# Kernel optimization log

Hardware: AMD Instinct MI355X
Metric: run time of the kernel (lower is better)

Reference implementation:

```python
import jax, jax.numpy as jnp
import numpy as np

B, T, D = 8, 1024, 1024
H = 16
HD = D // H
FF = 4 * D
EPS = 1e-5


def _ln(x, gamma, beta):
    # torch.var default is unbiased (ddof=1); MyLayerNorm intended normalization
    mean = jnp.mean(x, axis=-1, keepdims=True)
    var = jnp.var(x, axis=-1, keepdims=True, ddof=1)
    return (x - mean) / jnp.sqrt(var + EPS) * gamma + beta


def setup_inputs() -> dict:
    key = jax.random.key(0)
    ks = jax.random.split(key, 16)
    s = lambda k, shape, fan: jax.random.normal(k, shape, jnp.float32) * (fan ** -0.5)
    return {
        "x": jax.random.normal(ks[0], (B, T, D), jnp.float32),
        "Wq": s(ks[1], (D, D), D), "bq": jnp.zeros((D,), jnp.float32),
        "Wk": s(ks[2], (D, D), D), "bk": jnp.zeros((D,), jnp.float32),
        "Wv": s(ks[3], (D, D), D), "bv": jnp.zeros((D,), jnp.float32),
        "Wo": s(ks[4], (D, D), D), "bo": jnp.zeros((D,), jnp.float32),
        "W1": s(ks[5], (D, FF), D), "b1": jnp.zeros((FF,), jnp.float32),
        "W2": s(ks[6], (FF, D), FF), "b2": jnp.zeros((D,), jnp.float32),
        "g1": jnp.ones((D,), jnp.float32), "be1": jnp.zeros((D,), jnp.float32),
        "g2": jnp.ones((D,), jnp.float32), "be2": jnp.zeros((D,), jnp.float32),
    }


def reference(x, Wq, bq, Wk, bk, Wv, bv, Wo, bo, W1, b1, W2, b2, g1, be1, g2, be2):
    # pre-attention LN
    h = _ln(x, g1, be1)
    # batched QKV (equivalent to concatenated per-head Linears)
    q = (h @ Wq + bq).reshape(B, T, H, HD)
    k = (h @ Wk + bk).reshape(B, T, H, HD)
    v = (h @ Wv + bv).reshape(B, T, H, HD)
    att = jnp.einsum("bthd,bshd->bhts", q, k) * (HD ** -0.5)
    att = jax.nn.softmax(att, axis=-1)
    ctx = jnp.einsum("bhts,bshd->bthd", att, v).reshape(B, T, D)
    h = h + (ctx @ Wo + bo)
    # pre-FFN LN
    h2 = _ln(h, g2, be2)
    ff = jax.nn.gelu(h2 @ W1 + b1, approximate=False) @ W2 + b2
    return h2 + ff
```

## Files before the change

### kernel.cpp

```cpp
#include <hip/hip_runtime.h>
#include <hip/hip_bf16.h>

typedef unsigned short u16;
typedef __attribute__((ext_vector_type(8))) short bf16x8;
typedef __attribute__((ext_vector_type(4))) float floatx4;

__device__ __forceinline__ u16 f2b(float f) {
    union { float f; unsigned int u; } a; a.f = f;
    unsigned int u = a.u;
    unsigned int r = (u + 0x7fffu + ((u >> 16) & 1u)) >> 16;
    return (u16)r;
}
__device__ __forceinline__ float b2f(u16 v) {
    union { unsigned int u; float f; } a; a.u = ((unsigned int)v) << 16;
    return a.f;
}
__device__ __forceinline__ unsigned int cvt_pk_bf16(float lo, float hi) {
    unsigned int r;
    asm("v_cvt_pk_bf16_f32 %0, %1, %2" : "=v"(r) : "v"(lo), "v"(hi));
    return r;
}

__device__ __forceinline__ void gload_lds16(const void* g, void* l) {
    auto gp = (const __attribute__((address_space(1))) unsigned int*)g;
    auto lp = (__attribute__((address_space(3))) unsigned int*)l;
    __builtin_amdgcn_global_load_lds(gp, lp, 16, 0, 0);
}

__global__ __launch_bounds__(256) void k_ln_bf(const float* __restrict__ x,
                                               const float* __restrict__ g,
                                               const float* __restrict__ be,
                                               u16* __restrict__ yb) {
    const int row = blockIdx.x;
    const int t = threadIdx.x;
    const float4 xv = ((const float4*)(x + (size_t)row * 1024))[t];
    float s  = xv.x + xv.y + xv.z + xv.w;
    float ss = xv.x * xv.x + xv.y * xv.y + xv.z * xv.z + xv.w * xv.w;
    for (int m = 1; m < 64; m <<= 1) {
        s  += __shfl_xor(s, m);
        ss += __shfl_xor(ss, m);
    }
    __shared__ float sm[8];
    const int wave = t >> 6, lane = t & 63;
    if (lane == 0) { sm[wave] = s; sm[4 + wave] = ss; }
    __syncthreads();
    s  = sm[0] + sm[1] + sm[2] + sm[3];
    ss = sm[4] + sm[5] + sm[6] + sm[7];
    const float mean = s * (1.0f / 1024.0f);
    const float var  = (ss - 1024.0f * mean * mean) * (1.0f / 1023.0f);
    const float rstd = rsqrtf(var + 1e-5f);
    const float4 gv = ((const float4*)g)[t];
    const float4 bv = ((const float4*)be)[t];
    float4 y;
    y.x = (xv.x - mean) * rstd * gv.x + bv.x;
    y.y = (xv.y - mean) * rstd * gv.y + bv.y;
    y.z = (xv.z - mean) * rstd * gv.z + bv.z;
    y.w = (xv.w - mean) * rstd * gv.w + bv.w;
    uint2 pk;
    pk.x = (unsigned int)f2b(y.x) | ((unsigned int)f2b(y.y) << 16);
    pk.y = (unsigned int)f2b(y.z) | ((unsigned int)f2b(y.w) << 16);
    *(uint2*)(yb + (size_t)row * 1024 + t * 4) = pk;
}

__global__ __launch_bounds__(256) void k_tconv(const float* __restrict__ W,
                                               u16* __restrict__ Wt,
                                               int K, int N) {
    __shared__ float tile[32][33];
    const int n0 = blockIdx.x * 32, k0 = blockIdx.y * 32;
    const int tx = threadIdx.x, ty = threadIdx.y;
    for (int i = 0; i < 4; i++) {
        const int kr = ty + i * 8;
        tile[kr][tx] = W[(size_t)(k0 + kr) * N + n0 + tx];
    }
    __syncthreads();
    for (int i = 0; i < 4; i++) {
        const int nr = ty + i * 8;
        Wt[(size_t)(n0 + nr) * K + k0 + tx] = f2b(tile[tx][nr]);
    }
}

__global__ __launch_bounds__(256) void k_tconv4(const float* __restrict__ s0, u16* __restrict__ d0,
                                                const float* __restrict__ s1, u16* __restrict__ d1,
                                                const float* __restrict__ s2, u16* __restrict__ d2,
                                                const float* __restrict__ s3, u16* __restrict__ d3) {
    __shared__ float tile[32][33];
    const float* W; u16* Wt;
    switch (blockIdx.z) {
        case 0: W = s0; Wt = d0; break;
        case 1: W = s1; Wt = d1; break;
        case 2: W = s2; Wt = d2; break;
        default: W = s3; Wt = d3; break;
    }
    const int n0 = blockIdx.x * 32, k0 = blockIdx.y * 32;
    const int tx = threadIdx.x, ty = threadIdx.y;
    for (int i = 0; i < 4; i++) {
        const int kr = ty + i * 8;
        tile[kr][tx] = W[(size_t)(k0 + kr) * 1024 + n0 + tx];
    }
    __syncthreads();
    for (int i = 0; i < 4; i++) {
        const int nr = ty + i * 8;
        Wt[(size_t)(n0 + nr) * 1024 + k0 + tx] = f2b(tile[tx][nr]);
    }
}

__global__ __launch_bounds__(256) void k_vtrans(const u16* __restrict__ v,
                                                u16* __restrict__ vt) {
    __shared__ u16 tile[64][80];
    const int t = threadIdx.x;
    const int t0 = blockIdx.x * 64, hh = blockIdx.y, bb = blockIdx.z;
    const int r = t >> 2, c0 = (t & 3) * 16;
    const u16* src = v + ((size_t)(bb * 1024 + t0 + r)) * 1024 + hh * 64 + c0;
    *(uint4*)&tile[r][c0]     = *(const uint4*)src;
    *(uint4*)&tile[r][c0 + 8] = *(const uint4*)(src + 8);
    __syncthreads();
    const int d = t >> 2;
    u16* dst = vt + (((size_t)(bb * 16 + hh) * 64 + d)) * 1024 + t0 + c0;
    union { u16 s[8]; uint4 v4; } pk;
    for (int j = 0; j < 8; j++) pk.s[j] = tile[c0 + j][d];
    *(uint4*)dst = pk.v4;
    for (int j = 0; j < 8; j++) pk.s[j] = tile[c0 + 8 + j][d];
    *(uint4*)(dst + 8) = pk.v4;
}

template <bool GELU, bool RESID, bool WF32, bool WBF16, bool QKV = false>
__global__ __launch_bounds__(256) void k_gemm(const u16* __restrict__ A,
                                              const u16* __restrict__ Bt,
                                              const float* __restrict__ bias,
                                              const u16* __restrict__ residB,
                                              float* __restrict__ outF,
                                              u16* __restrict__ outB,
                                              int M, int N, int K,
                                              const float* __restrict__ bias2 = nullptr,
                                              const float* __restrict__ bias3 = nullptr) {
    __shared__ __align__(16) u16 S[16896];
    u16* As = S;
    u16* Bs = S + 8192;
    const int t = threadIdx.x;

    const int nb = gridDim.x;
    const int linear = blockIdx.y * nb + blockIdx.x;
    const int per = nb * 8;
    const int gg = linear / per, rr = linear % per;
    const int m0 = (gg * 8 + (rr & 7)) * 128;
    const int n0 = (rr >> 3) * 128;

    const int lane = t & 63, wave = t >> 6;
    const int wm = (wave >> 1) * 64, wn = (wave & 1) * 64;
    const int r16 = lane & 15, quad = lane >> 4;

    floatx4 acc[4][4];
    const floatx4 zero = {0.0f, 0.0f, 0.0f, 0.0f};
    for (int i = 0; i < 4; i++)
        for (int j = 0; j < 4; j++) acc[i][j] = zero;

    const u16* pa[4];
    const u16* pb[4];
    #pragma unroll
    for (int i = 0; i < 4; i++) {
        const int L = t + i * 256;
        const int row = L >> 3, col = L & 7;
        const int gcol = col ^ (row & 7);
        pa[i] = A  + (size_t)(m0 + row) * K + gcol * 8;
        pb[i] = Bt + (size_t)(n0 + row) * K + gcol * 8;
    }

    for (int kk = 0; kk < K; kk += 64) {
        #pragma unroll
        for (int i = 0; i < 4; i++) {
            gload_lds16(pa[i] + kk, As + (t + i * 256) * 8);
            gload_lds16(pb[i] + kk, Bs + (t + i * 256) * 8);
        }
        __syncthreads();

        #pragma unroll
        for (int ks = 0; ks < 2; ks++) {
            bf16x8 af[4], bfr[4];
            #pragma unroll
            for (int i = 0; i < 4; i++) {
                const int ra = wm + i * 16 + r16;
                af[i] = *(const bf16x8*)(As + ra * 64 + (((ks << 2) + quad) ^ (ra & 7)) * 8);
                const int rb = wn + i * 16 + r16;
                bfr[i] = *(const bf16x8*)(Bs + rb * 64 + (((ks << 2) + quad) ^ (rb & 7)) * 8);
            }
            #pragma unroll
            for (int mi = 0; mi < 4; mi++)
                #pragma unroll
                for (int ni = 0; ni < 4; ni++)
                    acc[mi][ni] = __builtin_amdgcn_mfma_f32_16x16x32_bf16(af[mi], bfr[ni], acc[mi][ni], 0, 0, 0);
        }
        __syncthreads();
    }

    const int sect = QKV ? (n0 >> 10) : 0;
    const float* bp = QKV ? (sect == 0 ? bias : (sect == 1 ? bias2 : bias3)) : bias;
    u16* outQ = QKV ? (outB + (size_t)sect * (8192ull * 1024ull)) : outB;

    if (WBF16) {
        u16 (*ct)[132] = (u16(*)[132])S;
        for (int mi = 0; mi < 4; mi++)
            for (int ni = 0; ni < 4; ni++) {
                const int col = wn + ni * 16 + r16;
                const int coln = QKV ? ((n0 + col) & 1023) : (n0 + col);
                const float bv = bp[coln];
                for (int r = 0; r < 4; r++) {
                    const int row = wm + mi * 16 + quad * 4 + r;
                    float v = acc[mi][ni][r] + bv;
                    if (GELU) v = 0.5f * v * (1.0f + erff(v * 0.70710678118654752f));
                    ct[row][col] = f2b(v);
                }
            }
        __syncthreads();
        const int orow = t >> 1, oc = (t & 1) * 64;
        const int grow = m0 + orow;
        u16* dst = QKV ? (outQ + (size_t)grow * 1024 + ((n0 + oc) & 1023))
                       : (outB + (size_t)grow * N + n0 + oc);
        #pragma unroll
        for (int j = 0; j < 8; j++)
            *(uint4*)(dst + j * 8) = *(const uint4*)&ct[orow][oc + j * 8];
    } else {
        for (int mi = 0; mi < 4; mi++)
            for (int ni = 0; ni < 4; ni++) {
                const int gcol = n0 + wn + ni * 16 + r16;
                const float bv = bias[gcol];
                for (int r = 0; r < 4; r++) {
                    const int grow = m0 + wm + mi * 16 + quad * 4 + r;
                    float v = acc[mi][ni][r] + bv;
                    if (GELU) v = 0.5f * v * (1.0f + erff(v * 0.70710678118654752f));
                    const size_t o = (size_t)grow * N + gcol;
                    if (RESID) v += b2f(residB[o]);
                    if (WF32) outF[o] = v;
                }
            }
    }
}

__global__ __launch_bounds__(256) void k_attn_mfma(const u16* __restrict__ q,
                                                   const u16* __restrict__ k,
                                                   const u16* __restrict__ vt,
                                                   u16* __restrict__ ctx) {
    __shared__ u16 Ks[2][64][40];
    __shared__ u16 Vs[2][64][40];
    __shared__ u16 Ps[2][64][40];
    const int t = threadIdx.x;
    const int lane = t & 63, wave = t >> 6;
    const int r16 = lane & 15, quad = lane >> 4;
    const int wq = wave * 16;
    const int bx = blockIdx.x;
    const int qt = bx & 15, hh = (bx >> 4) & 15, bb = bx >> 8;
    const size_t qk_base = ((size_t)bb * 1024) * 1024 + hh * 64;
    const size_t vt_base = ((size_t)(bb * 16 + hh) * 64) * 1024;
    const int q0 = qt * 64;
    const float C1 = 0.18033688011112042f;

    bf16x8 qf[2];
    {
        const u16* qp = q + qk_base + (size_t)(q0 + wq + r16) * 1024 + quad * 8;
        qf[0] = *(const bf16x8*)qp;
        qf[1] = *(const bf16x8*)(qp + 32);
    }

    const int srow = t >> 2, ch = t & 3;
    const int pnl = ch >> 1, soff = (ch & 1) * 16;
    const u16* gkb = k + qk_base + (size_t)srow * 1024 + ch * 16;
    const u16* gvb = vt + vt_base + (size_t)srow * 1024 + ch * 16;

    uint4 k0v = *(const uint4*)gkb;
    uint4 k1v = *(const uint4*)(gkb + 8);
    uint4 v0v = *(const uint4*)gvb;
    uint4 v1v = *(const uint4*)(gvb + 8);

    float m_i = -INFINITY, l_i = 0.0f;
    floatx4 acc_o[4];
    const floatx4 zero = {0.0f, 0.0f, 0.0f, 0.0f};
    for (int ni = 0; ni < 4; ni++) acc_o[ni] = zero;

    for (int st = 0; st < 16; st++) {
        *(uint4*)&Ks[pnl][srow][soff]     = k0v;
        *(uint4*)&Ks[pnl][srow][soff + 8] = k1v;
        *(uint4*)&Vs[pnl][srow][soff]     = v0v;
        *(uint4*)&Vs[pnl][srow][soff + 8] = v1v;
        __syncthreads();

        const int sn = (st + 1) & 15;
        const u16* gk = gkb + (size_t)sn * 65536;
        const u16* gv = gvb + sn * 64;
        const uint4 kn0 = *(const uint4*)gk;
        const uint4 kn1 = *(const uint4*)(gk + 8);
        const uint4 vn0 = *(const uint4*)gv;
        const uint4 vn1 = *(const uint4*)(gv + 8);

        floatx4 accs[4];
        for (int ni = 0; ni < 4; ni++) accs[ni] = zero;
        #pragma unroll
        for (int ks = 0; ks < 2; ks++) {
            #pragma unroll
            for (int ni = 0; ni < 4; ni++) {
                const bf16x8 kf = *(const bf16x8*)&Ks[ks][ni * 16 + r16][quad * 8];
                accs[ni] = __builtin_amdgcn_mfma_f32_16x16x32_bf16(kf, qf[ks], accs[ni], 0, 0, 0);
            }
        }

        float mx = -INFINITY;
        #pragma unroll
        for (int ni = 0; ni < 4; ni++)
            #pragma unroll
            for (int r = 0; r < 4; r++) mx = fmaxf(mx, accs[ni][r]);
        mx = fmaxf(mx, __shfl_xor(mx, 16));
        mx = fmaxf(mx, __shfl_xor(mx, 32));
        const float mn = fmaxf(m_i, mx);
        const float al = exp2f((m_i - mn) * C1);
        m_i = mn;
        const float negmc = -mn * C1;
        float ps = 0.0f;
        #pragma unroll
        for (int ni = 0; ni < 4; ni++) {
            const float p0 = exp2f(fmaf(accs[ni][0], C1, negmc));
            const float p1 = exp2f(fmaf(accs[ni][1], C1, negmc));
            const float p2 = exp2f(fmaf(accs[ni][2], C1, negmc));
            const float p3 = exp2f(fmaf(accs[ni][3], C1, negmc));
            ps += (p0 + p1) + (p2 + p3);
            uint2 w;
            w.x = cvt_pk_bf16(p0, p1);
            w.y = cvt_pk_bf16(p2, p3);
            *(uint2*)&Ps[ni >> 1][wq + r16][(ni & 1) * 16 + quad * 4] = w;
        }
        ps += __shfl_xor(ps, 16);
        ps += __shfl_xor(ps, 32);
        l_i = l_i * al + ps;
        #pragma unroll
        for (int r = 0; r < 4; r++) {
            const float alr = __shfl(al, quad * 4 + r);
            #pragma unroll
            for (int ni = 0; ni < 4; ni++) acc_o[ni][r] *= alr;
        }

        #pragma unroll
        for (int ks = 0; ks < 2; ks++) {
            const bf16x8 af = *(const bf16x8*)&Ps[ks][wq + r16][quad * 8];
            #pragma unroll
            for (int ni = 0; ni < 4; ni++) {
                const bf16x8 bf = *(const bf16x8*)&Vs[ks][ni * 16 + r16][quad * 8];
                acc_o[ni] = __builtin_amdgcn_mfma_f32_16x16x32_bf16(af, bf, acc_o[ni], 0, 0, 0);
            }
        }

        k0v = kn0; k1v = kn1; v0v = vn0; v1v = vn1;
        __syncthreads();
    }

    for (int r = 0; r < 4; r++) {
        const float linv = 1.0f / __shfl(l_i, quad * 4 + r);
        const size_t rowoff = qk_base + (size_t)(q0 + wq + quad * 4 + r) * 1024;
        for (int ni = 0; ni < 4; ni++)
            ctx[rowoff + ni * 16 + r16] = f2b(acc_o[ni][r] * linv);
    }
}

extern "C" void kernel_launch(void* const* d_in, const int* in_sizes, int n_in,
                              void* d_out, int out_size, void* d_ws, size_t ws_size,
                              hipStream_t stream) {
    const float* x   = (const float*)d_in[0];
    const float* Wq  = (const float*)d_in[1];
    const float* bq  = (const float*)d_in[2];
    const float* Wk  = (const float*)d_in[3];
    const float* bk  = (const float*)d_in[4];
    const float* Wv  = (const float*)d_in[5];
    const float* bv  = (const float*)d_in[6];
    const float* Wo  = (const float*)d_in[7];
    const float* bo  = (const float*)d_in[8];
    const float* W1  = (const float*)d_in[9];
    const float* b1  = (const float*)d_in[10];
    const float* W2  = (const float*)d_in[11];
    const float* b2  = (const float*)d_in[12];
    const float* g1  = (const float*)d_in[13];
    const float* be1 = (const float*)d_in[14];
    const float* g2  = (const float*)d_in[15];
    const float* be2 = (const float*)d_in[16];
    float* out = (float*)d_out;

    const size_t MB = 1ull << 20;
    char* ws = (char*)d_ws;
    u16*   h_b    = (u16*)(ws + 0);
    u16*   qkv_b  = (u16*)(ws + 16 * MB);
    u16*   q_b    = qkv_b;
    u16*   k_b    = (u16*)(ws + 32 * MB);
    u16*   v_b    = (u16*)(ws + 48 * MB);
    u16*   vt_b   = (u16*)(ws + 64 * MB);
    u16*   ctx_b  = (u16*)(ws + 80 * MB);
    float* hres   = (float*)(ws + 96 * MB);
    u16*   h2_b   = (u16*)(ws + 128 * MB);
    u16*   g_b    = (u16*)(ws + 16 * MB);
    u16*   wqkv_t = (u16*)(ws + 160 * MB);
    u16*   wo_t   = (u16*)(ws + 166 * MB);
    u16*   w1_t   = (u16*)(ws + 168 * MB);
    u16*   w2_t   = (u16*)(ws + 176 * MB);
    const int M = 8192, D = 1024, FF = 4096;
    const dim3 tb(32, 8);

    k_tconv4<<<dim3(32, 32, 4), tb, 0, stream>>>(Wq, wqkv_t,
                                                 Wk, wqkv_t + 1024 * 1024,
                                                 Wv, wqkv_t + 2 * 1024 * 1024,
                                                 Wo, wo_t);
    k_tconv<<<dim3(128, 32), tb, 0, stream>>>(W1, w1_t, D, FF);
    k_tconv<<<dim3(32, 128), tb, 0, stream>>>(W2, w2_t, FF, D);

    k_ln_bf<<<M, 256, 0, stream>>>(x, g1, be1, h_b);

    k_gemm<false, false, false, true, true><<<dim3(24, 64), 256, 0, stream>>>(
        h_b, wqkv_t, bq, nullptr, nullptr, qkv_b, M, 3072, D, bk, bv);

    k_vtrans<<<dim3(16, 16, 8), 256, 0, stream>>>(v_b, vt_b);

    k_attn_mfma<<<2048, 256, 0, stream>>>(q_b, k_b, vt_b, ctx_b);

    k_gemm<false, true, true, false><<<dim3(8, 64), 256, 0, stream>>>(
        ctx_b, wo_t, bo, h_b, hres, nullptr, M, D, D);

    k_ln_bf<<<M, 256, 0, stream>>>(hres, g2, be2, h2_b);

    k_gemm<true, false, false, true><<<dim3(32, 64), 256, 0, stream>>>(
        h2_b, w1_t, b1, nullptr, nullptr, g_b, M, FF, D);

    k_gemm<false, true, true, false><<<dim3(8, 64), 256, 0, stream>>>(
        g_b, w2_t, b2, h2_b, out, nullptr, M, D, FF);
}
```

Before: 575.8 us.

## Add 256x256-tile 512-thread GEMM for QKV and FFN1 projections

Adds a new GEMM kernel that uses 256x256 output tiles, 8 waves, and double-buffered 64-wide K stages loaded directly into LDS with an XOR swizzle. The inner loop splits MFMA work into four quadrant phases with explicit barriers and raised wave priority, and blocks are mapped in groups of 8 along M to improve L2 reuse. The QKV and W1+GELU projections switch to this kernel to raise arithmetic intensity per LDS and global load. In exchange it uses 128KB of LDS and many accumulator registers per thread, which limits occupancy to one block per CU.

```diff
diff --git a/kernel.cpp b/kernel.cpp
--- a/kernel.cpp
+++ b/kernel.cpp
@@ -25,6 +25,12 @@
     auto gp = (const __attribute__((address_space(1))) unsigned int*)g;
     auto lp = (__attribute__((address_space(3))) unsigned int*)l;
     __builtin_amdgcn_global_load_lds(gp, lp, 16, 0, 0);
+}
+
+__device__ __forceinline__ void sbar() {
+    __builtin_amdgcn_sched_barrier(0);
+    __builtin_amdgcn_s_barrier();
+    __builtin_amdgcn_sched_barrier(0);
 }
 
 __global__ __launch_bounds__(256) void k_ln_bf(const float* __restrict__ x,
@@ -232,6 +238,186 @@
                     if (WF32) outF[o] = v;
                 }
             }
+    }
+}
+
+template <bool GELU, bool QKV>
+__global__ __launch_bounds__(512) void k_gemm256(const u16* __restrict__ A,
+                                                 const u16* __restrict__ Bt,
+                                                 const float* __restrict__ bias,
+                                                 u16* __restrict__ outB,
+                                                 int M, int N, int K,
+                                                 const float* __restrict__ bias2 = nullptr,
+                                                 const float* __restrict__ bias3 = nullptr) {
+    __shared__ __align__(16) u16 S[65536];
+    const int t = threadIdx.x;
+    const int lane = t & 63, wave = t >> 6;
+    const int wm = wave >> 2, wn = wave & 3;
+    const int r16 = lane & 15, quad = lane >> 4;
+
+    const int nb = gridDim.x;
+    const int linear = blockIdx.y * nb + blockIdx.x;
+    const int per = nb * 8;
+    const int gg = linear / per, rr = linear % per;
+    const int m0 = (gg * 8 + (rr & 7)) * 256;
+    const int n0 = (rr >> 3) * 256;
+
+    floatx4 acc[8][4];
+    const floatx4 zero = {0.0f, 0.0f, 0.0f, 0.0f};
+    #pragma unroll
+    for (int i = 0; i < 8; i++)
+        #pragma unroll
+        for (int j = 0; j < 4; j++) acc[i][j] = zero;
+
+    int offA[4], offB[4];
+    #pragma unroll
+    for (int i = 0; i < 4; i++) {
+        const int L = t + i * 512;
+        const int row = L >> 3, col = L & 7;
+        const int gcol = col ^ (row & 7);
+        offA[i] = (m0 + row) * K + gcol * 8;
+        offB[i] = (n0 + row) * K + gcol * 8;
+    }
+
+    auto stage = [&](int buf, int kk) {
+        #pragma unroll
+        for (int i = 0; i < 4; i++) {
+            gload_lds16(A + offA[i] + kk, S + buf * 32768 + (t + i * 512) * 8);
+            gload_lds16(Bt + offB[i] + kk, S + 16384 + buf * 32768 + (t + i * 512) * 8);
+        }
+    };
+
+    const int NT = K >> 6;
+    stage(0, 0);
+    stage(1, 64);
+    asm volatile("s_waitcnt vmcnt(8)" ::: "memory");
+    sbar();
+
+    for (int kt = 0; kt < NT; kt++) {
+        const int cur = kt & 1;
+        const u16* As = S + cur * 32768;
+        const u16* Bs = S + 16384 + cur * 32768;
+
+        bf16x8 a1[2][4], a2[2][4], b1[2][2], b2[2][2];
+
+        #pragma unroll
+        for (int ks = 0; ks < 2; ks++)
+            #pragma unroll
+            for (int mi = 0; mi < 4; mi++) {
+                const int ra = wm * 128 + mi * 16 + r16;
+                a1[ks][mi] = *(const bf16x8*)(As + ra * 64 + (((ks << 2) + quad) ^ (ra & 7)) * 8);
+            }
+        #pragma unroll
+        for (int ks = 0; ks < 2; ks++)
+            #pragma unroll
+            for (int ni = 0; ni < 2; ni++) {
+                const int rb = wn * 64 + ni * 16 + r16;
+                b1[ks][ni] = *(const bf16x8*)(Bs + rb * 64 + (((ks << 2) + quad) ^ (rb & 7)) * 8);
+            }
+        sbar();
+        __builtin_amdgcn_s_setprio(1);
+        #pragma unroll
+        for (int ks = 0; ks < 2; ks++)
+            #pragma unroll
+            for (int mi = 0; mi < 4; mi++)
+                #pragma unroll
+                for (int ni = 0; ni < 2; ni++)
+                    acc[mi][ni] = __builtin_amdgcn_mfma_f32_16x16x32_bf16(a1[ks][mi], b1[ks][ni], acc[mi][ni], 0, 0, 0);
+        __builtin_amdgcn_s_setprio(0);
+
+        #pragma unroll
+        for (int ks = 0; ks < 2; ks++)
+            #pragma unroll
+            for (int mi = 0; mi < 4; mi++) {
+                const int ra = wm * 128 + 64 + mi * 16 + r16;
+                a2[ks][mi] = *(const bf16x8*)(As + ra * 64 + (((ks << 2) + quad) ^ (ra & 7)) * 8);
+            }
+        sbar();
+        __builtin_amdgcn_s_setprio(1);
+        #pragma unroll
+        for (int ks = 0; ks < 2; ks++)
+            #pragma unroll
+            for (int mi = 0; mi < 4; mi++)
+                #pragma unroll
+                for (int ni = 0; ni < 2; ni++)
+                    acc[4 + mi][ni] = __builtin_amdgcn_mfma_f32_16x16x32_bf16(a2[ks][mi], b1[ks][ni], acc[4 + mi][ni], 0, 0, 0);
+        __builtin_amdgcn_s_setprio(0);
+
+        #pragma unroll
+        for (int ks = 0; ks < 2; ks++)
+            #pragma unroll
+            for (int ni = 0; ni < 2; ni++) {
+                const int rb = wn * 64 + 32 + ni * 16 + r16;
+                b2[ks][ni] = *(const bf16x8*)(Bs + rb * 64 + (((ks << 2) + quad) ^ (rb & 7)) * 8);
+            }
+        sbar();
+        __builtin_amdgcn_s_setprio(1);
+        #pragma unroll
+        for (int ks = 0; ks < 2; ks++)
+            #pragma unroll
+            for (int mi = 0; mi < 4; mi++)
+                #pragma unroll
+                for (int ni = 0; ni < 2; ni++)
+                    acc[mi][2 + ni] = __builtin_amdgcn_mfma_f32_16x16x32_bf16(a1[ks][mi], b2[ks][ni], acc[mi][2 + ni], 0, 0, 0);
+        __builtin_amdgcn_s_setprio(0);
+
+        sbar();
+        __builtin_amdgcn_s_setprio(1);
+        #pragma unroll
+        for (int ks = 0; ks < 2; ks++)
+            #pragma unroll
+            for (int mi = 0; mi < 4; mi++)
+                #pragma unroll
+                for (int ni = 0; ni < 2; ni++)
+                    acc[4 + mi][2 + ni] = __builtin_amdgcn_mfma_f32_16x16x32_bf16(a2[ks][mi], b2[ks][ni], acc[4 + mi][2 + ni], 0, 0, 0);
+        __builtin_amdgcn_s_setprio(0);
+
+        sbar();
+        if (kt + 2 < NT) {
+            stage(cur, (kt + 2) << 6);
+            asm volatile("s_waitcnt vmcnt(8)" ::: "memory");
+        } else if (kt + 1 < NT) {
+            asm volatile("s_waitcnt vmcnt(0)" ::: "memory");
+        }
+        sbar();
+    }
+
+    const int sect = QKV ? (n0 >> 10) : 0;
+    const float* bp = QKV ? (sect == 0 ? bias : (sect == 1 ? bias2 : bias3)) : bias;
+    u16* outQ = QKV ? (outB + (size_t)sect * (8192ull * 1024ull)) : outB;
+
+    float bvv[4];
+    #pragma unroll
+    for (int ni = 0; ni < 4; ni++) {
+        const int col = wn * 64 + ni * 16 + r16;
+        bvv[ni] = bp[QKV ? ((n0 + col) & 1023) : (n0 + col)];
+    }
+    u16 (*ct)[260] = (u16(*)[260])S;
+    __syncthreads();
+    for (int mh = 0; mh < 2; mh++) {
+        if (wm == mh) {
+            #pragma unroll
+            for (int mi = 0; mi < 8; mi++)
+                #pragma unroll
+                for (int ni = 0; ni < 4; ni++) {
+                    const int col = wn * 64 + ni * 16 + r16;
+                    #pragma unroll
+                    for (int r = 0; r < 4; r++) {
+                        float v = acc[mi][ni][r] + bvv[ni];
+                        if (GELU) v = 0.5f * v * (1.0f + erff(v * 0.70710678118654752f));
+                        ct[mi * 16 + quad * 4 + r][col] = f2b(v);
+                    }
+                }
+        }
+        __syncthreads();
+        const int orow = t >> 2, oc = (t & 3) * 64;
+        const int grow = m0 + mh * 128 + orow;
+        u16* dst = QKV ? (outQ + (size_t)grow * 1024 + ((n0 + oc) & 1023))
+                       : (outB + (size_t)grow * N + n0 + oc);
+        #pragma unroll
+        for (int j = 0; j < 8; j++)
+            *(uint4*)(dst + j * 8) = *(const uint4*)&ct[orow][oc + j * 8];
+        __syncthreads();
     }
 }
 
@@ -407,8 +593,8 @@
 
     k_ln_bf<<<M, 256, 0, stream>>>(x, g1, be1, h_b);
 
-    k_gemm<false, false, false, true, true><<<dim3(24, 64), 256, 0, stream>>>(
-        h_b, wqkv_t, bq, nullptr, nullptr, qkv_b, M, 3072, D, bk, bv);
+    k_gemm256<false, true><<<dim3(12, 32), 512, 0, stream>>>(
+        h_b, wqkv_t, bq, qkv_b, M, 3072, D, bk, bv);
 
     k_vtrans<<<dim3(16, 16, 8), 256, 0, stream>>>(v_b, vt_b);
 
@@ -419,8 +605,8 @@
 
     k_ln_bf<<<M, 256, 0, stream>>>(hres, g2, be2, h2_b);
 
-    k_gemm<true, false, false, true><<<dim3(32, 64), 256, 0, stream>>>(
-        h2_b, w1_t, b1, nullptr, nullptr, g_b, M, FF, D);
+    k_gemm256<true, false><<<dim3(16, 32), 512, 0, stream>>>(
+        h2_b, w1_t, b1, g_b, M, FF, D);
 
     k_gemm<false, true, true, false><<<dim3(8, 64), 256, 0, stream>>>(
         g_b, w2_t, b2, h2_b, out, nullptr, M, D, FF);
```

After: 892.5 us. +55.0%, slower.
